# Kernel optimization log

Hardware: AMD Instinct MI355X
Metric: run time of the kernel (lower is better)

Reference implementation:

```python
import jax, jax.numpy as jnp
import numpy as np

V, D, NH, L, HID, E, K = 32000, 1024, 16, 2, 2048, 8, 2
B, S = 2, 1024
HD = D // NH
EPS = 1e-6
ROPE_BASE = 10000.0


def setup_inputs() -> dict:
    key = jax.random.key(0)
    ks = jax.random.split(key, 12)
    s = 0.02
    return {
        "tokens": jax.random.randint(ks[0], (B, S), 0, V),
        "embed": jax.random.normal(ks[1], (V, D), jnp.float32) * s,
        "attn_norm_w": jnp.ones((L, D), jnp.float32),
        "wq": jax.random.normal(ks[2], (L, D, D), jnp.float32) * s,
        "wk": jax.random.normal(ks[3], (L, D, D), jnp.float32) * s,
        "wv": jax.random.normal(ks[4], (L, D, D), jnp.float32) * s,
        "wo": jax.random.normal(ks[5], (L, D, D), jnp.float32) * s,
        "moe_norm_w": jnp.ones((L, D), jnp.float32),
        "router_w": jax.random.normal(ks[6], (L, E, D), jnp.float32) * s,
        "w1": jax.random.normal(ks[7], (L, E, D, HID), jnp.float32) * s,
        "w2": jax.random.normal(ks[8], (L, E, HID, D), jnp.float32) * s,
        "w3": jax.random.normal(ks[9], (L, E, D, HID), jnp.float32) * s,
        "final_norm_w": jnp.ones((D,), jnp.float32),
    }


def rmsnorm(x, w):
    var = jnp.mean(jnp.square(x), axis=-1, keepdims=True)
    return x * jax.lax.rsqrt(var + EPS) * w


def rope(x):  # x: [B, S, NH, HD], rotate-half convention
    half = HD // 2
    inv = ROPE_BASE ** (-jnp.arange(half, dtype=jnp.float32) / half)
    ang = jnp.arange(x.shape[1], dtype=jnp.float32)[:, None] * inv[None, :]  # [S, half]
    cos = jnp.cos(ang)[None, :, None, :]
    sin = jnp.sin(ang)[None, :, None, :]
    x1, x2 = x[..., :half], x[..., half:]
    return jnp.concatenate([x1 * cos - x2 * sin, x1 * sin + x2 * cos], axis=-1)


def attention(x, wq, wk, wv, wo):
    q = (x @ wq).reshape(B, S, NH, HD)
    k = (x @ wk).reshape(B, S, NH, HD)
    v = (x @ wv).reshape(B, S, NH, HD)
    q, k = rope(q), rope(k)
    scores = jnp.einsum("bqhd,bkhd->bhqk", q, k) / jnp.sqrt(jnp.float32(HD))
    mask = jnp.tril(jnp.ones((S, S), bool))
    scores = jnp.where(mask[None, None], scores, jnp.finfo(scores.dtype).min)
    attn = jax.nn.softmax(scores, axis=-1)
    ctx = jnp.einsum("bhqk,bkhd->bqhd", attn, v).reshape(B, S, D)
    return ctx @ wo


def moe(x, router_w, w1, w2, w3):
    flat = x.reshape(-1, D)                      # [T, D]
    T = flat.shape[0]
    logits = flat @ router_w.T                   # [T, E]
    topv, topi = jax.lax.top_k(logits, K)
    topw = jax.nn.softmax(topv, axis=-1)         # softmax over selected logits
    gates = jnp.zeros((T, E), flat.dtype).at[jnp.arange(T)[:, None], topi].set(topw)
    out = jnp.zeros_like(flat)
    for e in range(E):  # small fixed expert count; gates are exact-sparse so math == dispatch path
        y = (jax.nn.silu(flat @ w1[e]) * (flat @ w3[e])) @ w2[e]
        out = out + y * gates[:, e:e + 1]
    return out.reshape(x.shape)


def reference(tokens, embed, attn_norm_w, wq, wk, wv, wo, moe_norm_w,
              router_w, w1, w2, w3, final_norm_w):
    x = embed[tokens]  # [B, S, D]
    for l in range(L):
        x = x + attention(rmsnorm(x, attn_norm_w[l]), wq[l], wk[l], wv[l], wo[l])
        x = x + moe(rmsnorm(x, moe_norm_w[l]), router_w[l], w1[l], w2[l], w3[l])
    x = rmsnorm(x, final_norm_w)
    return x @ embed.T  # tied logits [B, S, V]
```

## Files before the change

kernel.cpp:

```cpp
#include <hip/hip_runtime.h>
#include <math.h>

typedef unsigned short u16;
typedef unsigned int u32;
typedef __attribute__((ext_vector_type(8))) short bf16x8;
typedef __attribute__((ext_vector_type(4))) float f32x4;

#define TOK 2048
#define SEQ 1024
#define DM 1024
#define NEXP 8
#define VOCAB 32000
#define NL 2
#define SLOTS 5120
#define APAD 40

__device__ __forceinline__ float bf2f(u16 v) {
  u32 u = ((u32)v) << 16; float f; __builtin_memcpy(&f, &u, 4); return f;
}
__device__ __forceinline__ u16 f2bf(float f) {
  u32 u; __builtin_memcpy(&u, &f, 4);
  u += 0x7fffu + ((u >> 16) & 1u);
  return (u16)(u >> 16);
}
__device__ __forceinline__ void split8(const float* v, u16* hi, u16* lo) {
#pragma unroll
  for (int j = 0; j < 8; j++) {
    hi[j] = f2bf(v[j]);
    lo[j] = f2bf(v[j] - bf2f(hi[j]));
  }
}

__global__ __launch_bounds__(256) void k_gather(const int* __restrict__ tok,
    const float* __restrict__ embed, float* __restrict__ x) {
  int t = blockIdx.x;
  ((float4*)(x + (long)t * DM))[threadIdx.x] =
      ((const float4*)(embed + (long)tok[t] * DM))[threadIdx.x];
}

__global__ __launch_bounds__(256) void k_f2bf(const float* __restrict__ in,
                                              u16* __restrict__ out, long n4) {
  long i = (long)blockIdx.x * 256 + threadIdx.x;
  long stride = (long)gridDim.x * 256;
  for (; i < n4; i += stride) {
    float4 v = ((const float4*)in)[i];
    ushort4 o;
    o.x = f2bf(v.x); o.y = f2bf(v.y); o.z = f2bf(v.z); o.w = f2bf(v.w);
    ((ushort4*)out)[i] = o;
  }
}

__global__ __launch_bounds__(256) void k_rmsnorm_hl(const float* __restrict__ x,
    const float* __restrict__ w, u16* __restrict__ ohi, u16* __restrict__ olo) {
  int t = blockIdx.x;
  float4 v = ((const float4*)(x + (long)t * DM))[threadIdx.x];
  float ss = v.x * v.x + v.y * v.y + v.z * v.z + v.w * v.w;
  for (int off = 32; off; off >>= 1) ss += __shfl_xor(ss, off);
  __shared__ float red[4];
  if ((threadIdx.x & 63) == 0) red[threadIdx.x >> 6] = ss;
  __syncthreads();
  float tot = red[0] + red[1] + red[2] + red[3];
  float sc = rsqrtf(tot * (1.0f / 1024.0f) + 1e-6f);
  float4 wv = ((const float4*)w)[threadIdx.x];
  float o[4] = {v.x * sc * wv.x, v.y * sc * wv.y, v.z * sc * wv.z, v.w * sc * wv.w};
  ushort4 hi, lo;
  hi.x = f2bf(o[0]); lo.x = f2bf(o[0] - bf2f(hi.x));
  hi.y = f2bf(o[1]); lo.y = f2bf(o[1] - bf2f(hi.y));
  hi.z = f2bf(o[2]); lo.z = f2bf(o[2] - bf2f(hi.z));
  hi.w = f2bf(o[3]); lo.w = f2bf(o[3] - bf2f(hi.w));
  ((ushort4*)(ohi + (long)t * DM))[threadIdx.x] = hi;
  ((ushort4*)(olo + (long)t * DM))[threadIdx.x] = lo;
}

__global__ __launch_bounds__(256) void k_rmsnorm_b(const float* __restrict__ x,
    const float* __restrict__ w, u16* __restrict__ out) {
  int t = blockIdx.x;
  float4 v = ((const float4*)(x + (long)t * DM))[threadIdx.x];
  float ss = v.x * v.x + v.y * v.y + v.z * v.z + v.w * v.w;
  for (int off = 32; off; off >>= 1) ss += __shfl_xor(ss, off);
  __shared__ float red[4];
  if ((threadIdx.x & 63) == 0) red[threadIdx.x >> 6] = ss;
  __syncthreads();
  float tot = red[0] + red[1] + red[2] + red[3];
  float sc = rsqrtf(tot * (1.0f / 1024.0f) + 1e-6f);
  float4 wv = ((const float4*)w)[threadIdx.x];
  ushort4 o;
  o.x = f2bf(v.x * sc * wv.x); o.y = f2bf(v.y * sc * wv.y);
  o.z = f2bf(v.z * sc * wv.z); o.w = f2bf(v.w * sc * wv.w);
  ((ushort4*)(out + (long)t * DM))[threadIdx.x] = o;
}

#define KP 72
#define VP 40
#define PP 36
__global__ __launch_bounds__(256) void k_attn(const float* __restrict__ qkv,
    u16* __restrict__ chi, u16* __restrict__ clo) {
  __shared__ u16 Ksh[32 * KP], Ksl[32 * KP];
  __shared__ u16 Vsh[64 * VP], Vsl[64 * VP];
  __shared__ float Ps[4][16 * PP];
  int qt = blockIdx.x;
  int bh = blockIdx.y;
  int b = bh >> 4, h = bh & 15;
  int tid = threadIdx.x, w = tid >> 6, lane = tid & 63;
  int lrow = lane & 15, lgrp = lane >> 4;
  int q0 = qt * 64;
  long qrow = (long)(b * SEQ + q0 + w * 16 + lrow);
  bf16x8 qh[2], ql[2];
#pragma unroll
  for (int dsl = 0; dsl < 2; dsl++) {
    const float* src = qkv + qrow * 3072 + h * 64 + dsl * 32 + lgrp * 8;
    float v[8];
    *(float4*)v = *(const float4*)src;
    *(float4*)(v + 4) = *(const float4*)(src + 4);
    u16 hi[8], lo[8];
    split8(v, hi, lo);
    qh[dsl] = *(bf16x8*)hi; ql[dsl] = *(bf16x8*)lo;
  }
  f32x4 cacc[4] = {};
  float mst[4], lst[4];
#pragma unroll
  for (int j = 0; j < 4; j++) { mst[j] = -__builtin_inff(); lst[j] = 0.0f; }
  int srow = tid >> 3, dchunk = (tid & 7) * 8;
  for (int s0 = 0; s0 < q0 + 64; s0 += 32) {
    long kvrow = (long)(b * SEQ + s0 + srow) * 3072 + h * 64;
    {
      const float* ksrc = qkv + kvrow + 1024 + dchunk;
      float v[8];
      *(float4*)v = *(const float4*)ksrc;
      *(float4*)(v + 4) = *(const float4*)(ksrc + 4);
#pragma unroll
      for (int j = 0; j < 8; j++) {
        u16 hi = f2bf(v[j]);
        Ksh[srow * KP + dchunk + j] = hi;
        Ksl[srow * KP + dchunk + j] = f2bf(v[j] - bf2f(hi));
      }
      const float* vsrc = qkv + kvrow + 2048 + dchunk;
      *(float4*)v = *(const float4*)vsrc;
      *(float4*)(v + 4) = *(const float4*)(vsrc + 4);
#pragma unroll
      for (int j = 0; j < 8; j++) {
        u16 hi = f2bf(v[j]);
        Vsh[(dchunk + j) * VP + srow] = hi;
        Vsl[(dchunk + j) * VP + srow] = f2bf(v[j] - bf2f(hi));
      }
    }
    __syncthreads();
    f32x4 sacc[2] = {};
#pragma unroll
    for (int sf = 0; sf < 2; sf++)
#pragma unroll
      for (int dsl = 0; dsl < 2; dsl++) {
        bf16x8 kh = *(const bf16x8*)(Ksh + (sf * 16 + lrow) * KP + dsl * 32 + lgrp * 8);
        bf16x8 kl = *(const bf16x8*)(Ksl + (sf * 16 + lrow) * KP + dsl * 32 + lgrp * 8);
        sacc[sf] = __builtin_amdgcn_mfma_f32_16x16x32_bf16(qh[dsl], kh, sacc[sf], 0, 0, 0);
        sacc[sf] = __builtin_amdgcn_mfma_f32_16x16x32_bf16(qh[dsl], kl, sacc[sf], 0, 0, 0);
        sacc[sf] = __builtin_amdgcn_mfma_f32_16x16x32_bf16(ql[dsl], kh, sacc[sf], 0, 0, 0);
      }
#pragma unroll
    for (int sf = 0; sf < 2; sf++)
#pragma unroll
      for (int j = 0; j < 4; j++) {
        int col = s0 + sf * 16 + lrow;
        int row = q0 + w * 16 + lgrp * 4 + j;
        float v = sacc[sf][j] * 0.125f;
        sacc[sf][j] = (col <= row) ? v : -1e30f;
      }
    float fac[4];
#pragma unroll
    for (int j = 0; j < 4; j++) {
      float mx = fmaxf(sacc[0][j], sacc[1][j]);
      for (int off = 1; off < 16; off <<= 1) mx = fmaxf(mx, __shfl_xor(mx, off));
      float mnew = fmaxf(mst[j], mx);
      float f = __expf(mst[j] - mnew);
      mst[j] = mnew;
      float p0 = __expf(sacc[0][j] - mnew);
      float p1 = __expf(sacc[1][j] - mnew);
      sacc[0][j] = p0; sacc[1][j] = p1;
      float ps = p0 + p1;
      for (int off = 1; off < 16; off <<= 1) ps += __shfl_xor(ps, off);
      lst[j] = lst[j] * f + ps;
      fac[j] = f;
    }
#pragma unroll
    for (int n = 0; n < 4; n++)
#pragma unroll
      for (int j = 0; j < 4; j++) cacc[n][j] *= fac[j];
#pragma unroll
    for (int sf = 0; sf < 2; sf++)
#pragma unroll
      for (int j = 0; j < 4; j++)
        Ps[w][(lgrp * 4 + j) * PP + sf * 16 + lrow] = sacc[sf][j];
    float pv[8];
#pragma unroll
    for (int j = 0; j < 8; j++) pv[j] = Ps[w][lrow * PP + lgrp * 8 + j];
    u16 phi[8], plo[8];
    split8(pv, phi, plo);
    bf16x8 ph = *(bf16x8*)phi, pl = *(bf16x8*)plo;
#pragma unroll
    for (int n = 0; n < 4; n++) {
      bf16x8 vh = *(const bf16x8*)(Vsh + (n * 16 + lrow) * VP + lgrp * 8);
      bf16x8 vl = *(const bf16x8*)(Vsl + (n * 16 + lrow) * VP + lgrp * 8);
      cacc[n] = __builtin_amdgcn_mfma_f32_16x16x32_bf16(ph, vh, cacc[n], 0, 0, 0);
      cacc[n] = __builtin_amdgcn_mfma_f32_16x16x32_bf16(ph, vl, cacc[n], 0, 0, 0);
      cacc[n] = __builtin_amdgcn_mfma_f32_16x16x32_bf16(pl, vh, cacc[n], 0, 0, 0);
    }
    __syncthreads();
  }
#pragma unroll
  for (int n = 0; n < 4; n++)
#pragma unroll
    for (int j = 0; j < 4; j++) {
      long t = (long)(b * SEQ + q0 + w * 16 + lgrp * 4 + j);
      float v = cacc[n][j] / lst[j];
      u16 hv = f2bf(v);
      chi[t * DM + h * 64 + n * 16 + lrow] = hv;
      clo[t * DM + h * 64 + n * 16 + lrow] = f2bf(v - bf2f(hv));
    }
}


__device__ __forceinline__ void stageB_tr(const float* __restrict__ B, int ldb,
    int k0, int n0, u16* Bh, u16* Bl, int tid, int split) {
#pragma unroll
  for (int ph = 0; ph < 2; ph++) {
    int c = tid + 256 * ph;
    int nr = c & 127;
    int ks = c >> 7;
    const float* src = B + (long)(k0 + ks * 8) * ldb + n0 + nr;
    float v[8];
#pragma unroll
    for (int j = 0; j < 8; j++) v[j] = src[(long)j * ldb];
    u16 hi[8];
#pragma unroll
    for (int j = 0; j < 8; j++) hi[j] = f2bf(v[j]);
    *(uint4*)(Bh + nr * APAD + ks * 8) = *(uint4*)hi;
    if (split) {
      u16 lo[8];
#pragma unroll
      for (int j = 0; j < 8; j++) lo[j] = f2bf(v[j] - bf2f(hi[j]));
      *(uint4*)(Bl + nr * APAD + ks * 8) = *(uint4*)lo;
    }
  }
}

__device__ __forceinline__ void stageA_cp(const u16* __restrict__ Ahi,
    const u16* __restrict__ Alo, long ldk, long m0, int k0,
    u16* Ah, u16* Al, int tid, int split) {
#pragma unroll
  for (int ph = 0; ph < 2; ph++) {
    int c = tid + 256 * ph;
    int row = c >> 2, kc = c & 3;
    long off = (m0 + row) * ldk + k0 + kc * 8;
    *(uint4*)(Ah + row * APAD + kc * 8) = *(const uint4*)(Ahi + off);
    if (split) *(uint4*)(Al + row * APAD + kc * 8) = *(const uint4*)(Alo + off);
  }
}

__global__ __launch_bounds__(256) void k_wo(
    const u16* __restrict__ Ahi, const u16* __restrict__ Alo,
    const float* __restrict__ B, float* __restrict__ C) {
  __shared__ u16 Ah[128 * APAD], Al[128 * APAD], Bh[128 * APAD], Bl[128 * APAD];
  int m0 = blockIdx.y * 128;
  int n0 = blockIdx.x * 128;
  int tid = threadIdx.x, lane = tid & 63, w = tid >> 6;
  int wr = w >> 1, wc = w & 1, lrow = lane & 15, lgrp = lane >> 4;
  f32x4 acc[4][4] = {};
  for (int k0 = 0; k0 < 1024; k0 += 32) {
    stageA_cp(Ahi, Alo, DM, m0, k0, Ah, Al, tid, 1);
    stageB_tr(B, 1024, k0, n0, Bh, Bl, tid, 1);
    __syncthreads();
    bf16x8 ah[4], bh[4], al[4], bl[4];
#pragma unroll
    for (int i = 0; i < 4; i++) {
      ah[i] = *(const bf16x8*)(Ah + (wr * 64 + i * 16 + lrow) * APAD + lgrp * 8);
      al[i] = *(const bf16x8*)(Al + (wr * 64 + i * 16 + lrow) * APAD + lgrp * 8);
      bh[i] = *(const bf16x8*)(Bh + (wc * 64 + i * 16 + lrow) * APAD + lgrp * 8);
      bl[i] = *(const bf16x8*)(Bl + (wc * 64 + i * 16 + lrow) * APAD + lgrp * 8);
    }
#pragma unroll
    for (int i = 0; i < 4; i++)
#pragma unroll
      for (int j = 0; j < 4; j++) {
        acc[i][j] = __builtin_amdgcn_mfma_f32_16x16x32_bf16(ah[i], bh[j], acc[i][j], 0, 0, 0);
        acc[i][j] = __builtin_amdgcn_mfma_f32_16x16x32_bf16(ah[i], bl[j], acc[i][j], 0, 0, 0);
        acc[i][j] = __builtin_amdgcn_mfma_f32_16x16x32_bf16(al[i], bh[j], acc[i][j], 0, 0, 0);
      }
    __syncthreads();
  }
#pragma unroll
  for (int i = 0; i < 4; i++)
#pragma unroll
    for (int j = 0; j < 4; j++) {
      int col = n0 + wc * 64 + j * 16 + lrow;
#pragma unroll
      for (int jj = 0; jj < 4; jj++) {
        int r = m0 + wr * 64 + i * 16 + lgrp * 4 + jj;
        C[(long)r * DM + col] += acc[i][j][jj];
      }
    }
}

__global__ __launch_bounds__(256) void k_gemm_qkv(
    const u16* __restrict__ Ahi, const u16* __restrict__ Alo,
    const float* __restrict__ Bq, const float* __restrict__ Bk,
    const float* __restrict__ Bv, float* __restrict__ C) {
  __shared__ u16 Ah[128 * APAD], Al[128 * APAD], Bh[128 * APAD], Bl[128 * APAD];
  int m0 = blockIdx.y * 128;
  int nb = blockIdx.x;
  const float* B = (nb < 8) ? Bq : (nb < 16) ? Bk : Bv;
  int bn0 = (nb & 7) * 128;
  int tid = threadIdx.x, lane = tid & 63, w = tid >> 6;
  int wr = w >> 1, wc = w & 1, lrow = lane & 15, lgrp = lane >> 4;
  f32x4 acc[4][4] = {};
  for (int k0 = 0; k0 < 1024; k0 += 32) {
    stageA_cp(Ahi, Alo, DM, m0, k0, Ah, Al, tid, 1);
    stageB_tr(B, 1024, k0, bn0, Bh, Bl, tid, 1);
    __syncthreads();
    bf16x8 ah[4], bh[4], al[4], bl[4];
#pragma unroll
    for (int i = 0; i < 4; i++) {
      ah[i] = *(const bf16x8*)(Ah + (wr * 64 + i * 16 + lrow) * APAD + lgrp * 8);
      al[i] = *(const bf16x8*)(Al + (wr * 64 + i * 16 + lrow) * APAD + lgrp * 8);
      bh[i] = *(const bf16x8*)(Bh + (wc * 64 + i * 16 + lrow) * APAD + lgrp * 8);
      bl[i] = *(const bf16x8*)(Bl + (wc * 64 + i * 16 + lrow) * APAD + lgrp * 8);
    }
#pragma unroll
    for (int i = 0; i < 4; i++)
#pragma unroll
      for (int j = 0; j < 4; j++) {
        acc[i][j] = __builtin_amdgcn_mfma_f32_16x16x32_bf16(ah[i], bh[j], acc[i][j], 0, 0, 0);
        acc[i][j] = __builtin_amdgcn_mfma_f32_16x16x32_bf16(ah[i], bl[j], acc[i][j], 0, 0, 0);
        acc[i][j] = __builtin_amdgcn_mfma_f32_16x16x32_bf16(al[i], bh[j], acc[i][j], 0, 0, 0);
      }
    __syncthreads();
  }
  if (nb < 16) {
    float inv1 = exp2f((float)lrow * (-13.287712379549449f / 32.0f));
    float inv2 = exp2f((float)(lrow + 16) * (-13.287712379549449f / 32.0f));
#pragma unroll
    for (int i = 0; i < 4; i++)
#pragma unroll
      for (int jj = 0; jj < 4; jj++) {
        int r = m0 + wr * 64 + i * 16 + lgrp * 4 + jj;
        float s = (float)(r & (SEQ - 1));
        float sn1, cs1, sn2, cs2;
        sincosf(s * inv1, &sn1, &cs1);
        sincosf(s * inv2, &sn2, &cs2);
        float q1 = acc[i][0][jj], q2 = acc[i][2][jj];
        acc[i][0][jj] = q1 * cs1 - q2 * sn1;
        acc[i][2][jj] = q1 * sn1 + q2 * cs1;
        float p1 = acc[i][1][jj], p2 = acc[i][3][jj];
        acc[i][1][jj] = p1 * cs2 - p2 * sn2;
        acc[i][3][jj] = p1 * sn2 + p2 * cs2;
      }
  }
#pragma unroll
  for (int i = 0; i < 4; i++)
#pragma unroll
    for (int j = 0; j < 4; j++) {
      int col = nb * 128 + wc * 64 + j * 16 + lrow;
#pragma unroll
      for (int jj = 0; jj < 4; jj++) {
        int r = m0 + wr * 64 + i * 16 + lgrp * 4 + jj;
        C[(long)r * 3072 + col] = acc[i][j][jj];
      }
    }
}

template <int SPLIT>
__global__ __launch_bounds__(256) void k_w13(
    const u16* __restrict__ Ahi, const u16* __restrict__ Alo,
    const float* __restrict__ W1, const float* __restrict__ W3,
    const int* __restrict__ lists, const int* __restrict__ counts,
    const int* __restrict__ aoff,
    float* __restrict__ h13) {
  int m0 = blockIdx.y * 128;
  int e = -1;
#pragma unroll
  for (int i = 0; i < NEXP; i++)
    if (m0 >= aoff[i] && m0 < aoff[i + 1]) e = i;
  if (e < 0) return;
  int lr0 = m0 - aoff[e];
  int Mc = counts[e];
  if (lr0 >= Mc) return;
  int nb = blockIdx.x;
  const float* B = ((nb < 16) ? W1 : W3) + (size_t)e * 1024 * 2048;
  int bn0 = (nb & 15) * 128;
  const int* lst = lists + e * TOK;
  __shared__ u16 Ah[128 * APAD], Bh[128 * APAD];
  __shared__ u16 Al[SPLIT ? 128 * APAD : 1], Bl[SPLIT ? 128 * APAD : 1];
  int tid = threadIdx.x, lane = tid & 63, w = tid >> 6;
  int wr = w >> 1, wc = w & 1, lrow = lane & 15, lgrp = lane >> 4;
  f32x4 acc[4][4] = {};
  for (int k0 = 0; k0 < 1024; k0 += 32) {
#pragma unroll
    for (int ph = 0; ph < 2; ph++) {
      int c = tid + 256 * ph;
      int row = c >> 2, kc = c & 3;
      uint4 vh = make_uint4(0, 0, 0, 0), vl = make_uint4(0, 0, 0, 0);
      if (lr0 + row < Mc) {
        long off = (long)lst[lr0 + row] * DM + k0 + kc * 8;
        vh = *(const uint4*)(Ahi + off);
        if (SPLIT) vl = *(const uint4*)(Alo + off);
      }
      *(uint4*)(Ah + row * APAD + kc * 8) = vh;
      if (SPLIT) *(uint4*)(Al + row * APAD + kc * 8) = vl;
    }
    stageB_tr(B, 2048, k0, bn0, Bh, Bl, tid, SPLIT);
    __syncthreads();
    bf16x8 ah[4], bh[4];
#pragma unroll
    for (int i = 0; i < 4; i++) {
      ah[i] = *(const bf16x8*)(Ah + (wr * 64 + i * 16 + lrow) * APAD + lgrp * 8);
      bh[i] = *(const bf16x8*)(Bh + (wc * 64 + i * 16 + lrow) * APAD + lgrp * 8);
    }
#pragma unroll
    for (int i = 0; i < 4; i++)
#pragma unroll
      for (int j = 0; j < 4; j++)
        acc[i][j] = __builtin_amdgcn_mfma_f32_16x16x32_bf16(ah[i], bh[j], acc[i][j], 0, 0, 0);
    if (SPLIT) {
      bf16x8 al[4], bl[4];
#pragma unroll
      for (int i = 0; i < 4; i++) {
        al[i] = *(const bf16x8*)(Al + (wr * 64 + i * 16 + lrow) * APAD + lgrp * 8);
        bl[i] = *(const bf16x8*)(Bl + (wc * 64 + i * 16 + lrow) * APAD + lgrp * 8);
      }
#pragma unroll
      for (int i = 0; i < 4; i++)
#pragma unroll
        for (int j = 0; j < 4; j++) {
          acc[i][j] = __builtin_amdgcn_mfma_f32_16x16x32_bf16(ah[i], bl[j], acc[i][j], 0, 0, 0);
          acc[i][j] = __builtin_amdgcn_mfma_f32_16x16x32_bf16(al[i], bh[j], acc[i][j], 0, 0, 0);
        }
    }
    __syncthreads();
  }
#pragma unroll
  for (int i = 0; i < 4; i++)
#pragma unroll
    for (int j = 0; j < 4; j++) {
      int col = nb * 128 + wc * 64 + j * 16 + lrow;
#pragma unroll
      for (int jj = 0; jj < 4; jj++) {
        int rl = wr * 64 + i * 16 + lgrp * 4 + jj;
        if (lr0 + rl >= Mc) continue;
        h13[(long)(m0 + rl) * 4096 + col] = acc[i][j][jj];
      }
    }
}

__global__ __launch_bounds__(256) void k_silu(const float* __restrict__ h13,
    const int* __restrict__ counts, const int* __restrict__ aoff,
    u16* __restrict__ hhi, u16* __restrict__ hlo) {
  int g = blockIdx.x;
  int e = -1;
#pragma unroll
  for (int i = 0; i < NEXP; i++)
    if (g >= aoff[i] && g < aoff[i + 1]) e = i;
  if (e < 0 || g - aoff[e] >= counts[e]) return;
  const float4* a = (const float4*)(h13 + (long)g * 4096);
  const float4* b = (const float4*)(h13 + (long)g * 4096 + 2048);
  for (int c = threadIdx.x; c < 512; c += 256) {
    float4 x1 = a[c], x3 = b[c];
    float o[4];
    o[0] = x1.x / (1.0f + __expf(-x1.x)) * x3.x;
    o[1] = x1.y / (1.0f + __expf(-x1.y)) * x3.y;
    o[2] = x1.z / (1.0f + __expf(-x1.z)) * x3.z;
    o[3] = x1.w / (1.0f + __expf(-x1.w)) * x3.w;
    ushort4 hi, lo;
    hi.x = f2bf(o[0]); lo.x = f2bf(o[0] - bf2f(hi.x));
    hi.y = f2bf(o[1]); lo.y = f2bf(o[1] - bf2f(hi.y));
    hi.z = f2bf(o[2]); lo.z = f2bf(o[2] - bf2f(hi.z));
    hi.w = f2bf(o[3]); lo.w = f2bf(o[3] - bf2f(hi.w));
    ((ushort4*)(hhi + (long)g * 2048))[c] = hi;
    ((ushort4*)(hlo + (long)g * 2048))[c] = lo;
  }
}

template <int SPLIT>
__global__ __launch_bounds__(256) void k_w2(
    const u16* __restrict__ Ahi, const u16* __restrict__ Alo,
    const float* __restrict__ W2,
    const int* __restrict__ counts, const int* __restrict__ aoff,
    float* __restrict__ y) {
  int m0 = blockIdx.y * 128;
  int e = -1;
#pragma unroll
  for (int i = 0; i < NEXP; i++)
    if (m0 >= aoff[i] && m0 < aoff[i + 1]) e = i;
  if (e < 0) return;
  int lr0 = m0 - aoff[e];
  int Mc = counts[e];
  if (lr0 >= Mc) return;
  const float* B = W2 + (size_t)e * 2048 * 1024;
  int n0 = blockIdx.x * 128;
  __shared__ u16 Ah[128 * APAD], Bh[128 * APAD];
  __shared__ u16 Al[SPLIT ? 128 * APAD : 1], Bl[SPLIT ? 128 * APAD : 1];
  int tid = threadIdx.x, lane = tid & 63, w = tid >> 6;
  int wr = w >> 1, wc = w & 1, lrow = lane & 15, lgrp = lane >> 4;
  f32x4 acc[4][4] = {};
  for (int k0 = 0; k0 < 2048; k0 += 32) {
    stageA_cp(Ahi, Alo, 2048, m0, k0, Ah, Al, tid, SPLIT);
    stageB_tr(B, 1024, k0, n0, Bh, Bl, tid, SPLIT);
    __syncthreads();
    bf16x8 ah[4], bh[4];
#pragma unroll
    for (int i = 0; i < 4; i++) {
      ah[i] = *(const bf16x8*)(Ah + (wr * 64 + i * 16 + lrow) * APAD + lgrp * 8);
      bh[i] = *(const bf16x8*)(Bh + (wc * 64 + i * 16 + lrow) * APAD + lgrp * 8);
    }
#pragma unroll
    for (int i = 0; i < 4; i++)
#pragma unroll
      for (int j = 0; j < 4; j++)
        acc[i][j] = __builtin_amdgcn_mfma_f32_16x16x32_bf16(ah[i], bh[j], acc[i][j], 0, 0, 0);
    if (SPLIT) {
      bf16x8 al[4], bl[4];
#pragma unroll
      for (int i = 0; i < 4; i++) {
        al[i] = *(const bf16x8*)(Al + (wr * 64 + i * 16 + lrow) * APAD + lgrp * 8);
        bl[i] = *(const bf16x8*)(Bl + (wc * 64 + i * 16 + lrow) * APAD + lgrp * 8);
      }
#pragma unroll
      for (int i = 0; i < 4; i++)
#pragma unroll
        for (int j = 0; j < 4; j++) {
          acc[i][j] = __builtin_amdgcn_mfma_f32_16x16x32_bf16(ah[i], bl[j], acc[i][j], 0, 0, 0);
          acc[i][j] = __builtin_amdgcn_mfma_f32_16x16x32_bf16(al[i], bh[j], acc[i][j], 0, 0, 0);
        }
    }
    __syncthreads();
  }
#pragma unroll
  for (int i = 0; i < 4; i++)
#pragma unroll
    for (int j = 0; j < 4; j++) {
      int col = n0 + wc * 64 + j * 16 + lrow;
#pragma unroll
      for (int jj = 0; jj < 4; jj++) {
        int rl = wr * 64 + i * 16 + lgrp * 4 + jj;
        if (lr0 + rl >= Mc) continue;
        y[(long)(m0 + rl) * DM + col] = acc[i][j][jj];
      }
    }
}

__global__ __launch_bounds__(256) void k_combine(const float* __restrict__ y,
    const int* __restrict__ aoff, const int* __restrict__ tok_e,
    const int* __restrict__ tok_pos, const float* __restrict__ tok_gate,
    float* __restrict__ x) {
  int t = blockIdx.x;
  float4 acc = ((float4*)(x + (long)t * DM))[threadIdx.x];
#pragma unroll
  for (int j = 0; j < 2; j++) {
    int e = tok_e[t * 2 + j];
    long g = aoff[e] + tok_pos[t * 2 + j];
    float gt = tok_gate[t * 2 + j];
    float4 yv = ((const float4*)(y + g * DM))[threadIdx.x];
    acc.x += gt * yv.x; acc.y += gt * yv.y;
    acc.z += gt * yv.z; acc.w += gt * yv.w;
  }
  ((float4*)(x + (long)t * DM))[threadIdx.x] = acc;
}

__global__ __launch_bounds__(512) void k_logits(
    const u16* __restrict__ A, const u16* __restrict__ Bt,
    float* __restrict__ C) {
  __shared__ u16 As[256 * APAD];
  __shared__ u16 Bs[128 * APAD];
  int bid = blockIdx.x;
  int xcd = bid & 7, rank = bid >> 3;
  int bx = xcd * 32 + (rank >> 3);
  int by = rank & 7;
  if (bx >= VOCAB / 128) return;
  int m0 = by * 256, n0 = bx * 128;
  int tid = threadIdx.x, lane = tid & 63, w = tid >> 6;
  int wr = w >> 1, wc = w & 1;
  int lrow = lane & 15, lgrp = lane >> 4;
  f32x4 acc[4][4] = {};
  for (int k0 = 0; k0 < 1024; k0 += 32) {
#pragma unroll
    for (int ph = 0; ph < 2; ph++) {
      int c = tid + 512 * ph;
      int row = c >> 2, kc = c & 3;
      *(uint4*)(As + row * APAD + kc * 8) =
          *(const uint4*)(A + (long)(m0 + row) * 1024 + k0 + kc * 8);
    }
    {
      int row = tid >> 2, kc = tid & 3;
      *(uint4*)(Bs + row * APAD + kc * 8) =
          *(const uint4*)(Bt + (long)(n0 + row) * 1024 + k0 + kc * 8);
    }
    __syncthreads();
    bf16x8 af[4], bfr[4];
#pragma unroll
    for (int i = 0; i < 4; i++) {
      af[i] = *(const bf16x8*)(As + (wr * 64 + i * 16 + lrow) * APAD + lgrp * 8);
      bfr[i] = *(const bf16x8*)(Bs + (wc * 64 + i * 16 + lrow) * APAD + lgrp * 8);
    }
#pragma unroll
    for (int i = 0; i < 4; i++)
#pragma unroll
      for (int j = 0; j < 4; j++)
        acc[i][j] = __builtin_amdgcn_mfma_f32_16x16x32_bf16(af[i], bfr[j], acc[i][j], 0, 0, 0);
    __syncthreads();
  }
#pragma unroll
  for (int i = 0; i < 4; i++)
#pragma unroll
    for (int j = 0; j < 4; j++) {
      int col = n0 + wc * 64 + j * 16 + lrow;
#pragma unroll
      for (int jj = 0; jj < 4; jj++) {
        int r = m0 + wr * 64 + i * 16 + lgrp * 4 + jj;
        C[(long)r * VOCAB + col] = acc[i][j][jj];
      }
    }
}

__global__ __launch_bounds__(256) void k_router(const float* __restrict__ x,
    const float* __restrict__ nw, const float* __restrict__ rw,
    int* __restrict__ counts, int* __restrict__ lists,
    int* __restrict__ tok_e, int* __restrict__ tok_pos,
    float* __restrict__ tok_gate) {
  int t = blockIdx.x * 4 + (threadIdx.x >> 6);
  int lane = threadIdx.x & 63;
  const float* xr = x + (long)t * DM;
  float ss = 0.0f;
  float p[8] = {0, 0, 0, 0, 0, 0, 0, 0};
  for (int i = 0; i < 16; i++) {
    int d = lane + 64 * i;
    float xv = xr[d];
    ss += xv * xv;
    float xw = xv * nw[d];
#pragma unroll
    for (int e = 0; e < 8; e++) p[e] += xw * rw[e * DM + d];
  }
  for (int off = 32; off; off >>= 1) ss += __shfl_xor(ss, off);
#pragma unroll
  for (int e = 0; e < 8; e++)
    for (int off = 32; off; off >>= 1) p[e] += __shfl_xor(p[e], off);
  if (lane == 0) {
    float sc = rsqrtf(ss * (1.0f / 1024.0f) + 1e-6f);
    int e0 = 0, e1 = -1;
    float v0 = -__builtin_inff(), v1 = -__builtin_inff();
    for (int e = 0; e < 8; e++) {
      float pe = p[e] * sc;
      if (pe > v0) { v1 = v0; e1 = e0; v0 = pe; e0 = e; }
      else if (pe > v1) { v1 = pe; e1 = e; }
    }
    float w0 = 1.0f / (1.0f + expf(v1 - v0));
    int pos0 = atomicAdd(&counts[e0], 1);
    lists[e0 * TOK + pos0] = t;
    tok_e[t * 2] = e0; tok_pos[t * 2] = pos0; tok_gate[t * 2] = w0;
    int pos1 = atomicAdd(&counts[e1], 1);
    lists[e1 * TOK + pos1] = t;
    tok_e[t * 2 + 1] = e1; tok_pos[t * 2 + 1] = pos1; tok_gate[t * 2 + 1] = 1.0f - w0;
  }
}

__global__ void k_offsets(const int* __restrict__ counts, int* __restrict__ aoff) {
  if (threadIdx.x == 0 && blockIdx.x == 0) {
    int a = 0;
    for (int e = 0; e < NEXP; e++) {
      aoff[e] = a;
      a += (counts[e] + 127) & ~127;
    }
    aoff[NEXP] = a;
  }
}

extern "C" void kernel_launch(void* const* d_in, const int* in_sizes, int n_in,
                              void* d_out, int out_size, void* d_ws, size_t ws_size,
                              hipStream_t stream) {
  (void)in_sizes; (void)n_in; (void)out_size; (void)ws_size;
  const int* tokens = (const int*)d_in[0];
  const float* embed = (const float*)d_in[1];
  const float* attn_nw = (const float*)d_in[2];
  const float* wq = (const float*)d_in[3];
  const float* wk = (const float*)d_in[4];
  const float* wv = (const float*)d_in[5];
  const float* wo = (const float*)d_in[6];
  const float* moe_nw = (const float*)d_in[7];
  const float* rw = (const float*)d_in[8];
  const float* w1 = (const float*)d_in[9];
  const float* w2 = (const float*)d_in[10];
  const float* w3 = (const float*)d_in[11];
  const float* fin_nw = (const float*)d_in[12];
  float* out = (float*)d_out;

  char* ob = (char*)d_out;
  auto carve = [&](size_t bytes) { char* r = ob; ob += (bytes + 255) & ~(size_t)255; return r; };
  float* qkv    = (float*)carve((size_t)TOK * 3072 * 4);
  u16*   ctx_hi = (u16*)carve((size_t)TOK * DM * 2);
  u16*   ctx_lo = (u16*)carve((size_t)TOK * DM * 2);
  float* x      = (float*)carve((size_t)TOK * DM * 4);
  float* h13    = (float*)carve((size_t)SLOTS * 4096 * 4);
  u16*   hb_hi  = (u16*)carve((size_t)SLOTS * 2048 * 2);
  u16*   hb_lo  = (u16*)carve((size_t)SLOTS * 2048 * 2);
  float* y      = (float*)carve((size_t)SLOTS * 1024 * 4);
  int*   counts  = (int*)carve(NEXP * 4);
  int*   aoff    = (int*)carve((NEXP + 1) * 4);
  int*   lists   = (int*)carve((size_t)NEXP * TOK * 4);
  int*   tok_e   = (int*)carve((size_t)TOK * 2 * 4);
  int*   tok_pos = (int*)carve((size_t)TOK * 2 * 4);
  float* tok_gate= (float*)carve((size_t)TOK * 2 * 4);
  char* wp = (char*)d_ws;
  auto wcarve = [&](size_t bytes) { char* r = wp; wp += (bytes + 255) & ~(size_t)255; return r; };
  u16* xn_hi = (u16*)wcarve((size_t)TOK * DM * 2);
  u16* xn_lo = (u16*)wcarve((size_t)TOK * DM * 2);
  u16* xnb   = (u16*)wcarve((size_t)TOK * DM * 2);
  u16* embB  = (u16*)wcarve((size_t)VOCAB * DM * 2);

  k_f2bf<<<4096, 256, 0, stream>>>(embed, embB, (long)VOCAB * DM / 4);
  k_gather<<<TOK, 256, 0, stream>>>(tokens, embed, x);

  for (int l = 0; l < NL; l++) {
    k_rmsnorm_hl<<<TOK, 256, 0, stream>>>(x, attn_nw + (size_t)l * DM, xn_hi, xn_lo);
    k_gemm_qkv<<<dim3(24, 16), 256, 0, stream>>>(xn_hi, xn_lo,
        wq + (size_t)l * DM * DM, wk + (size_t)l * DM * DM, wv + (size_t)l * DM * DM, qkv);
    k_attn<<<dim3(16, 32), 256, 0, stream>>>(qkv, ctx_hi, ctx_lo);
    k_wo<<<dim3(8, 16), 256, 0, stream>>>(ctx_hi, ctx_lo, wo + (size_t)l * DM * DM, x);

    hipMemsetAsync(counts, 0, NEXP * 4, stream);
    k_router<<<TOK / 4, 256, 0, stream>>>(x, moe_nw + (size_t)l * DM,
        rw + (size_t)l * NEXP * DM, counts, lists, tok_e, tok_pos, tok_gate);
    k_offsets<<<1, 64, 0, stream>>>(counts, aoff);
    k_rmsnorm_hl<<<TOK, 256, 0, stream>>>(x, moe_nw + (size_t)l * DM, xn_hi, xn_lo);
    if (l < NL - 1) {
      k_w13<1><<<dim3(32, SLOTS / 128), 256, 0, stream>>>(xn_hi, xn_lo,
          w1 + (size_t)l * NEXP * DM * 2048, w3 + (size_t)l * NEXP * DM * 2048,
          lists, counts, aoff, h13);
      k_silu<<<SLOTS, 256, 0, stream>>>(h13, counts, aoff, hb_hi, hb_lo);
      k_w2<1><<<dim3(8, SLOTS / 128), 256, 0, stream>>>(hb_hi, hb_lo,
          w2 + (size_t)l * NEXP * 2048 * DM, counts, aoff, y);
    } else {
      k_w13<0><<<dim3(32, SLOTS / 128), 256, 0, stream>>>(xn_hi, xn_lo,
          w1 + (size_t)l * NEXP * DM * 2048, w3 + (size_t)l * NEXP * DM * 2048,
          lists, counts, aoff, h13);
      k_silu<<<SLOTS, 256, 0, stream>>>(h13, counts, aoff, hb_hi, hb_lo);
      k_w2<0><<<dim3(8, SLOTS / 128), 256, 0, stream>>>(hb_hi, hb_lo,
          w2 + (size_t)l * NEXP * 2048 * DM, counts, aoff, y);
    }
    k_combine<<<TOK, 256, 0, stream>>>(y, aoff, tok_e, tok_pos, tok_gate, x);
  }
  k_rmsnorm_b<<<TOK, 256, 0, stream>>>(x, fin_nw, xnb);
  k_logits<<<2048, 512, 0, stream>>>(xnb, embB, out);
}
```

Measured before the change: 1.467 ms.

## Remap block IDs for XCD-aware L2 locality and double-buffer logits GEMM

Flattens the 2D grids of the attention, QKV, Wo, W13 and W2 kernels into 1D grids and remaps block IDs so that blocks landing on the same XCD share weight columns or heads, aiming to improve L2 reuse across the chiplets. Separately, the logits GEMM gets two shared-memory buffers with register prefetch of the next K tile, overlapping global loads with MFMA work and halving the barriers per K step. The cost is more LDS use in the logits kernel and an index mapping that depends on the hard-coded grid sizes.

Result: no change. 1.459 ms, median of 2 (-0.5%).

```diff
diff --git a/kernel.cpp b/kernel.cpp
--- a/kernel.cpp
+++ b/kernel.cpp
@@ -98,8 +98,10 @@
   __shared__ u16 Ksh[32 * KP], Ksl[32 * KP];
   __shared__ u16 Vsh[64 * VP], Vsl[64 * VP];
   __shared__ float Ps[4][16 * PP];
-  int qt = blockIdx.x;
-  int bh = blockIdx.y;
+  int bid = blockIdx.x;
+  int xcd = bid & 7, r = bid >> 3;
+  int bh = xcd * 4 + (r >> 4);
+  int qt = r & 15;
   int b = bh >> 4, h = bh & 15;
   int tid = threadIdx.x, w = tid >> 6, lane = tid & 63;
   int lrow = lane & 15, lgrp = lane >> 4;
@@ -260,8 +262,9 @@
     const u16* __restrict__ Ahi, const u16* __restrict__ Alo,
     const float* __restrict__ B, float* __restrict__ C) {
   __shared__ u16 Ah[128 * APAD], Al[128 * APAD], Bh[128 * APAD], Bl[128 * APAD];
-  int m0 = blockIdx.y * 128;
-  int n0 = blockIdx.x * 128;
+  int bid = blockIdx.x;
+  int n0 = (bid & 7) * 128;
+  int m0 = (bid >> 3) * 128;
   int tid = threadIdx.x, lane = tid & 63, w = tid >> 6;
   int wr = w >> 1, wc = w & 1, lrow = lane & 15, lgrp = lane >> 4;
   f32x4 acc[4][4] = {};
@@ -305,8 +308,10 @@
     const float* __restrict__ Bq, const float* __restrict__ Bk,
     const float* __restrict__ Bv, float* __restrict__ C) {
   __shared__ u16 Ah[128 * APAD], Al[128 * APAD], Bh[128 * APAD], Bl[128 * APAD];
-  int m0 = blockIdx.y * 128;
-  int nb = blockIdx.x;
+  int bid = blockIdx.x;
+  int xcd = bid & 7, r = bid >> 3;
+  int nb = xcd * 3 + r / 16;
+  int m0 = (r & 15) * 128;
   const float* B = (nb < 8) ? Bq : (nb < 16) ? Bk : Bv;
   int bn0 = (nb & 7) * 128;
   int tid = threadIdx.x, lane = tid & 63, w = tid >> 6;
@@ -341,8 +346,8 @@
     for (int i = 0; i < 4; i++)
 #pragma unroll
       for (int jj = 0; jj < 4; jj++) {
-        int r = m0 + wr * 64 + i * 16 + lgrp * 4 + jj;
-        float s = (float)(r & (SEQ - 1));
+        int rr = m0 + wr * 64 + i * 16 + lgrp * 4 + jj;
+        float s = (float)(rr & (SEQ - 1));
         float sn1, cs1, sn2, cs2;
         sincosf(s * inv1, &sn1, &cs1);
         sincosf(s * inv2, &sn2, &cs2);
@@ -361,8 +366,8 @@
       int col = nb * 128 + wc * 64 + j * 16 + lrow;
 #pragma unroll
       for (int jj = 0; jj < 4; jj++) {
-        int r = m0 + wr * 64 + i * 16 + lgrp * 4 + jj;
-        C[(long)r * 3072 + col] = acc[i][j][jj];
+        int rr = m0 + wr * 64 + i * 16 + lgrp * 4 + jj;
+        C[(long)rr * 3072 + col] = acc[i][j][jj];
       }
     }
 }
@@ -374,7 +379,10 @@
     const int* __restrict__ lists, const int* __restrict__ counts,
     const int* __restrict__ aoff,
     float* __restrict__ h13) {
-  int m0 = blockIdx.y * 128;
+  int bid = blockIdx.x;
+  int xcd = bid & 7, r = bid >> 3;
+  int nb = xcd * 4 + r / 40;
+  int m0 = (r % 40) * 128;
   int e = -1;
 #pragma unroll
   for (int i = 0; i < NEXP; i++)
@@ -383,7 +391,6 @@
   int lr0 = m0 - aoff[e];
   int Mc = counts[e];
   if (lr0 >= Mc) return;
-  int nb = blockIdx.x;
   const float* B = ((nb < 16) ? W1 : W3) + (size_t)e * 1024 * 2048;
   int bn0 = (nb & 15) * 128;
   const int* lst = lists + e * TOK;
@@ -484,7 +491,9 @@
     const float* __restrict__ W2,
     const int* __restrict__ counts, const int* __restrict__ aoff,
     float* __restrict__ y) {
-  int m0 = blockIdx.y * 128;
+  int bid = blockIdx.x;
+  int n0 = (bid & 7) * 128;
+  int m0 = (bid >> 3) * 128;
   int e = -1;
 #pragma unroll
   for (int i = 0; i < NEXP; i++)
@@ -494,7 +503,6 @@
   int Mc = counts[e];
   if (lr0 >= Mc) return;
   const float* B = W2 + (size_t)e * 2048 * 1024;
-  int n0 = blockIdx.x * 128;
   __shared__ u16 Ah[128 * APAD], Bh[128 * APAD];
   __shared__ u16 Al[SPLIT ? 128 * APAD : 1], Bl[SPLIT ? 128 * APAD : 1];
   int tid = threadIdx.x, lane = tid & 63, w = tid >> 6;
@@ -564,11 +572,26 @@
   ((float4*)(x + (long)t * DM))[threadIdx.x] = acc;
 }
 
+__device__ __forceinline__ void logits_mma(const u16* As, const u16* Bs,
+    f32x4 (&acc)[4][4], int wr, int wc, int lrow, int lgrp) {
+  bf16x8 af[4], bfr[4];
+#pragma unroll
+  for (int i = 0; i < 4; i++) {
+    af[i] = *(const bf16x8*)(As + (wr * 64 + i * 16 + lrow) * APAD + lgrp * 8);
+    bfr[i] = *(const bf16x8*)(Bs + (wc * 64 + i * 16 + lrow) * APAD + lgrp * 8);
+  }
+#pragma unroll
+  for (int i = 0; i < 4; i++)
+#pragma unroll
+    for (int j = 0; j < 4; j++)
+      acc[i][j] = __builtin_amdgcn_mfma_f32_16x16x32_bf16(af[i], bfr[j], acc[i][j], 0, 0, 0);
+}
+
 __global__ __launch_bounds__(512) void k_logits(
     const u16* __restrict__ A, const u16* __restrict__ Bt,
     float* __restrict__ C) {
-  __shared__ u16 As[256 * APAD];
-  __shared__ u16 Bs[128 * APAD];
+  __shared__ u16 AsA[256 * APAD], BsA[128 * APAD];
+  __shared__ u16 AsB[256 * APAD], BsB[128 * APAD];
   int bid = blockIdx.x;
   int xcd = bid & 7, rank = bid >> 3;
   int bx = xcd * 32 + (rank >> 3);
@@ -578,32 +601,42 @@
   int tid = threadIdx.x, lane = tid & 63, w = tid >> 6;
   int wr = w >> 1, wc = w & 1;
   int lrow = lane & 15, lgrp = lane >> 4;
+  int arow = tid >> 2, akc = tid & 3;
   f32x4 acc[4][4] = {};
-  for (int k0 = 0; k0 < 1024; k0 += 32) {
-#pragma unroll
-    for (int ph = 0; ph < 2; ph++) {
-      int c = tid + 512 * ph;
-      int row = c >> 2, kc = c & 3;
-      *(uint4*)(As + row * APAD + kc * 8) =
-          *(const uint4*)(A + (long)(m0 + row) * 1024 + k0 + kc * 8);
-    }
+  const u16* Ap = A + (long)(m0 + arow) * 1024 + akc * 8;
+  const u16* Ap2 = A + (long)(m0 + arow + 128) * 1024 + akc * 8;
+  const u16* Bp = Bt + (long)(n0 + arow) * 1024 + akc * 8;
+  uint4 a0 = *(const uint4*)(Ap);
+  uint4 a1 = *(const uint4*)(Ap2);
+  uint4 b0 = *(const uint4*)(Bp);
+  *(uint4*)(AsA + arow * APAD + akc * 8) = a0;
+  *(uint4*)(AsA + (arow + 128) * APAD + akc * 8) = a1;
+  *(uint4*)(BsA + arow * APAD + akc * 8) = b0;
+  __syncthreads();
+  for (int kt = 0; kt < 32; kt += 2) {
     {
-      int row = tid >> 2, kc = tid & 3;
-      *(uint4*)(Bs + row * APAD + kc * 8) =
-          *(const uint4*)(Bt + (long)(n0 + row) * 1024 + k0 + kc * 8);
-    }
-    __syncthreads();
-    bf16x8 af[4], bfr[4];
-#pragma unroll
-    for (int i = 0; i < 4; i++) {
-      af[i] = *(const bf16x8*)(As + (wr * 64 + i * 16 + lrow) * APAD + lgrp * 8);
-      bfr[i] = *(const bf16x8*)(Bs + (wc * 64 + i * 16 + lrow) * APAD + lgrp * 8);
-    }
-#pragma unroll
-    for (int i = 0; i < 4; i++)
-#pragma unroll
-      for (int j = 0; j < 4; j++)
-        acc[i][j] = __builtin_amdgcn_mfma_f32_16x16x32_bf16(af[i], bfr[j], acc[i][j], 0, 0, 0);
+      int k0 = (kt + 1) * 32;
+      a0 = *(const uint4*)(Ap + k0);
+      a1 = *(const uint4*)(Ap2 + k0);
+      b0 = *(const uint4*)(Bp + k0);
+    }
+    logits_mma(AsA, BsA, acc, wr, wc, lrow, lgrp);
+    *(uint4*)(AsB + arow * APAD + akc * 8) = a0;
+    *(uint4*)(AsB + (arow + 128) * APAD + akc * 8) = a1;
+    *(uint4*)(BsB + arow * APAD + akc * 8) = b0;
+    __syncthreads();
+    if (kt + 2 < 32) {
+      int k0 = (kt + 2) * 32;
+      a0 = *(const uint4*)(Ap + k0);
+      a1 = *(const uint4*)(Ap2 + k0);
+      b0 = *(const uint4*)(Bp + k0);
+    }
+    logits_mma(AsB, BsB, acc, wr, wc, lrow, lgrp);
+    if (kt + 2 < 32) {
+      *(uint4*)(AsA + arow * APAD + akc * 8) = a0;
+      *(uint4*)(AsA + (arow + 128) * APAD + akc * 8) = a1;
+      *(uint4*)(BsA + arow * APAD + akc * 8) = b0;
+    }
     __syncthreads();
   }
 #pragma unroll
@@ -718,10 +751,10 @@
 
   for (int l = 0; l < NL; l++) {
     k_rmsnorm_hl<<<TOK, 256, 0, stream>>>(x, attn_nw + (size_t)l * DM, xn_hi, xn_lo);
-    k_gemm_qkv<<<dim3(24, 16), 256, 0, stream>>>(xn_hi, xn_lo,
+    k_gemm_qkv<<<384, 256, 0, stream>>>(xn_hi, xn_lo,
         wq + (size_t)l * DM * DM, wk + (size_t)l * DM * DM, wv + (size_t)l * DM * DM, qkv);
-    k_attn<<<dim3(16, 32), 256, 0, stream>>>(qkv, ctx_hi, ctx_lo);
-    k_wo<<<dim3(8, 16), 256, 0, stream>>>(ctx_hi, ctx_lo, wo + (size_t)l * DM * DM, x);
+    k_attn<<<512, 256, 0, stream>>>(qkv, ctx_hi, ctx_lo);
+    k_wo<<<128, 256, 0, stream>>>(ctx_hi, ctx_lo, wo + (size_t)l * DM * DM, x);
 
     hipMemsetAsync(counts, 0, NEXP * 4, stream);
     k_router<<<TOK / 4, 256, 0, stream>>>(x, moe_nw + (size_t)l * DM,
@@ -729,18 +762,18 @@
     k_offsets<<<1, 64, 0, stream>>>(counts, aoff);
     k_rmsnorm_hl<<<TOK, 256, 0, stream>>>(x, moe_nw + (size_t)l * DM, xn_hi, xn_lo);
     if (l < NL - 1) {
-      k_w13<1><<<dim3(32, SLOTS / 128), 256, 0, stream>>>(xn_hi, xn_lo,
+      k_w13<1><<<1280, 256, 0, stream>>>(xn_hi, xn_lo,
           w1 + (size_t)l * NEXP * DM * 2048, w3 + (size_t)l * NEXP * DM * 2048,
           lists, counts, aoff, h13);
       k_silu<<<SLOTS, 256, 0, stream>>>(h13, counts, aoff, hb_hi, hb_lo);
-      k_w2<1><<<dim3(8, SLOTS / 128), 256, 0, stream>>>(hb_hi, hb_lo,
+      k_w2<1><<<320, 256, 0, stream>>>(hb_hi, hb_lo,
           w2 + (size_t)l * NEXP * 2048 * DM, counts, aoff, y);
     } else {
-      k_w13<0><<<dim3(32, SLOTS / 128), 256, 0, stream>>>(xn_hi, xn_lo,
+      k_w13<0><<<1280, 256, 0, stream>>>(xn_hi, xn_lo,
           w1 + (size_t)l * NEXP * DM * 2048, w3 + (size_t)l * NEXP * DM * 2048,
           lists, counts, aoff, h13);
       k_silu<<<SLOTS, 256, 0, stream>>>(h13, counts, aoff, hb_hi, hb_lo);
-      k_w2<0><<<dim3(8, SLOTS / 128), 256, 0, stream>>>(hb_hi, hb_lo,
+      k_w2<0><<<320, 256, 0, stream>>>(hb_hi, hb_lo,
           w2 + (size_t)l * NEXP * 2048 * DM, counts, aoff, y);
     }
     k_combine<<<TOK, 256, 0, stream>>>(y, aoff, tok_e, tok_pos, tok_gate, x);
```
